# Optimization experiments

Measured on AMD Instinct MI355X. Metric: run time of the kernel, lower is better.

The kernel has to match this reference:

```python
import jax, jax.numpy as jnp
import numpy as np

D_MODEL = 1024
NHEAD = 16
D_K = D_MODEL // NHEAD
EPS_ATTN = 1e-6
EPS_LN = 1e-5


def _linear(k, fan_in, fan_out):
    k1, k2 = jax.random.split(k)
    bound = 1.0 / np.sqrt(fan_in)
    W = jax.random.uniform(k1, (fan_out, fan_in), jnp.float32, -bound, bound)
    b = jax.random.uniform(k2, (fan_out,), jnp.float32, -bound, bound)
    return W, b


def setup_inputs() -> dict:
    key = jax.random.key(0)
    ks = jax.random.split(key, 8)
    src = jax.random.normal(ks[0], (4096, 4, D_MODEL), jnp.float32)
    Wq, bq = _linear(ks[1], D_MODEL, D_MODEL)
    Wk, bk = _linear(ks[2], D_MODEL, D_MODEL)
    Wv, bv = _linear(ks[3], D_MODEL, D_MODEL)
    Wo, bo = _linear(ks[4], D_MODEL, D_MODEL)
    W1, b1 = _linear(ks[5], D_MODEL, 2 * D_MODEL)
    W2, b2 = _linear(ks[6], 2 * D_MODEL, D_MODEL)
    g1 = jnp.ones((D_MODEL,), jnp.float32)
    be1 = jnp.zeros((D_MODEL,), jnp.float32)
    g2 = jnp.ones((D_MODEL,), jnp.float32)
    be2 = jnp.zeros((D_MODEL,), jnp.float32)
    return {"src": src, "Wq": Wq, "bq": bq, "Wk": Wk, "bk": bk, "Wv": Wv, "bv": bv,
            "Wo": Wo, "bo": bo, "W1": W1, "b1": b1, "W2": W2, "b2": b2,
            "g1": g1, "be1": be1, "g2": g2, "be2": be2}


def _layernorm(x, g, b):
    mu = jnp.mean(x, axis=-1, keepdims=True)
    var = jnp.mean(jnp.square(x - mu), axis=-1, keepdims=True)
    return (x - mu) * jax.lax.rsqrt(var + EPS_LN) * g + b


def reference(src, Wq, bq, Wk, bk, Wv, bv, Wo, bo, W1, b1, W2, b2, g1, be1, g2, be2):
    S, B, D = src.shape
    Q = src @ Wq.T + bq  # [S,B,D]
    K = src @ Wk.T + bk
    V = src @ Wv.T + bv
    # split heads: [S,B,H,dk]
    Q = Q.reshape(S, B, NHEAD, D_K)
    K = K.reshape(S, B, NHEAD, D_K)
    V = V.reshape(S, B, NHEAD, D_K)
    phiQ = jax.nn.elu(Q) + 1.0
    phiK = jax.nn.elu(K) + 1.0
    # context per (batch, head): [B,H,dk,dk]
    context = jnp.einsum('sbhd,sbhe->bhde', phiK, V)
    out = jnp.einsum('sbhd,bhde->sbhe', phiQ, context)
    denom = jnp.einsum('sbhd,bhd->sbh', phiQ, phiK.sum(axis=0))
    out = out / (denom[..., None] + EPS_ATTN)
    attn = out.reshape(S, B, D)  # concat heads
    out = attn @ Wo.T + bo  # dropout = identity (eval)
    out = _layernorm(src + out, g1, be1)
    ffn = jax.nn.relu(out @ W1.T + b1) @ W2.T + b2
    out = _layernorm(out + ffn, g2, be2)
    return out
```

## Files before the change

kernel.cpp:

```cpp
#include <hip/hip_runtime.h>
#include <hip/hip_bf16.h>

typedef __hip_bfloat16 bf16;
typedef __attribute__((ext_vector_type(4))) float floatx4;
typedef __attribute__((ext_vector_type(8))) short shortx8;

#define MFMA16(a, b, c) __builtin_amdgcn_mfma_f32_16x16x32_bf16(a, b, c, 0, 0, 0)

__device__ __forceinline__ void gll16(const bf16* g, void* l) {
  __builtin_amdgcn_global_load_lds((const __attribute__((address_space(1))) unsigned int*)g,
                                   (__attribute__((address_space(3))) unsigned int*)l,
                                   16, 0, 0);
}

__device__ __forceinline__ float b2f(short s) {
  return __bfloat162float(__builtin_bit_cast(bf16, (unsigned short)s));
}
__device__ __forceinline__ short f2b(float f) {
  return __builtin_bit_cast(short, __float2bfloat16(f));
}

__global__ __launch_bounds__(256) void f2b_all(
    const float* __restrict__ src, const float* __restrict__ Wq,
    const float* __restrict__ Wk, const float* __restrict__ Wv,
    const float* __restrict__ Wo, const float* __restrict__ W1,
    const float* __restrict__ W2, bf16* __restrict__ src_bf,
    bf16* __restrict__ Wq_b, bf16* __restrict__ Wk_b, bf16* __restrict__ Wv_b,
    bf16* __restrict__ Wo_b, bf16* __restrict__ W1_b, bf16* __restrict__ W2_b) {
  const int blk = blockIdx.x;
  const float* in;
  bf16* out;
  int off;
  if (blk < 16384)      { in = src; out = src_bf; off = blk; }
  else if (blk < 17408) { in = Wq; out = Wq_b; off = blk - 16384; }
  else if (blk < 18432) { in = Wk; out = Wk_b; off = blk - 17408; }
  else if (blk < 19456) { in = Wv; out = Wv_b; off = blk - 18432; }
  else if (blk < 20480) { in = Wo; out = Wo_b; off = blk - 19456; }
  else if (blk < 22528) { in = W1; out = W1_b; off = blk - 20480; }
  else                  { in = W2; out = W2_b; off = blk - 22528; }
  const int i = (off * 256 + threadIdx.x) * 4;
  float4 v = *(const float4*)(in + i);
  ushort4 u;
  u.x = (unsigned short)f2b(v.x);
  u.y = (unsigned short)f2b(v.y);
  u.z = (unsigned short)f2b(v.z);
  u.w = (unsigned short)f2b(v.w);
  *(ushort4*)(out + i) = u;
}

template <int EPI>
__global__ __launch_bounds__(256, 2) void gemm_nt(
    const bf16* __restrict__ A, const bf16* __restrict__ Bw,
    const float* __restrict__ bias0, const float* __restrict__ bias1,
    const float* __restrict__ bias2, const float* __restrict__ resf,
    const bf16* __restrict__ resb, void* __restrict__ out0,
    void* __restrict__ out1, void* __restrict__ out2, const int M,
    const int K) {
  __shared__ __align__(16) char smem[24576];
  bf16* sA = (bf16*)smem;
  bf16* sB = (bf16*)(smem + 8192);
  bf16* cep = (bf16*)smem;
#define CEP(gg, rr, cc) cep[(((gg)*16 + (rr)) * 268) + (cc)]
  const int tid = threadIdx.x;
  const int lane = tid & 63, wave = tid >> 6;
  const int wm = wave & 1, wn = wave >> 1;
  const int bm = blockIdx.x, bn = blockIdx.y;
  floatx4 acc[4][8] = {};
  const int srow = tid >> 2;
  const int schunk = (tid & 3) ^ ((srow >> 1) & 3);
  const bf16* Ab = A + (size_t)(bm * 128 + srow) * K + schunk * 8;
  const bf16* Bb = Bw + (size_t)(bn * 256 + srow) * K + schunk * 8;
  const int woff = wave * 1024;
  const int frow = lane & 15;
  const int fks = (((lane >> 4) ^ ((frow >> 1) & 3))) << 3;
  const size_t rK = (size_t)64 * K;

  for (int k0 = 0; k0 < K; k0 += 32) {
    __syncthreads();
    gll16(Ab + k0, smem + woff);
    gll16(Ab + rK + k0, smem + 4096 + woff);
    gll16(Bb + k0, smem + 8192 + woff);
    gll16(Bb + rK + k0, smem + 12288 + woff);
    gll16(Bb + 2 * rK + k0, smem + 16384 + woff);
    gll16(Bb + 3 * rK + k0, smem + 20480 + woff);
    __syncthreads();
    shortx8 af[4], bfr[8];
#pragma unroll
    for (int i = 0; i < 4; i++)
      af[i] = *(const shortx8*)&sA[(wm * 64 + i * 16 + frow) * 32 + fks];
#pragma unroll
    for (int j = 0; j < 8; j++)
      bfr[j] = *(const shortx8*)&sB[(wn * 128 + j * 16 + frow) * 32 + fks];
#pragma unroll
    for (int i = 0; i < 4; i++)
#pragma unroll
      for (int j = 0; j < 8; j++)
        acc[i][j] = MFMA16(af[i], bfr[j], acc[i][j]);
  }

  const float* bptr = bias0;
  bf16* ob = (bf16*)out0;
  int colbase = bn * 256;
  int phi = 0;
  if (EPI == 4) {
    const int sel = bn >> 2;
    bptr = (sel == 0) ? bias0 : (sel == 1) ? bias1 : bias2;
    ob = (bf16*)((sel == 0) ? out0 : (sel == 1) ? out1 : out2);
    colbase = (bn & 3) * 256;
    phi = (sel < 2);
  }
  const int e = lane & 15, q4 = (lane >> 4) << 2;
  float bj[8];
#pragma unroll
  for (int j = 0; j < 8; j++) bj[j] = bptr[colbase + wn * 128 + j * 16 + e];

  const int g = tid >> 7;
  const int rowl = (tid >> 3) & 15;
  const int cch = (tid & 7) * 8;

#pragma unroll
  for (int i = 0; i < 4; i++) {
    __syncthreads();
#pragma unroll
    for (int j = 0; j < 8; j++) {
#pragma unroll
      for (int r = 0; r < 4; r++) {
        float v = acc[i][j][r] + bj[j];
        if (EPI == 4 && phi) v = v > 0.f ? v + 1.f : __expf(v);
        if (EPI == 2) v = fmaxf(v, 0.f);
        CEP(wm, q4 + r, wn * 128 + j * 16 + e) = __builtin_bit_cast(bf16, f2b(v));
      }
    }
    __syncthreads();
    const int grow = bm * 128 + g * 64 + i * 16 + rowl;
#pragma unroll
    for (int c = 0; c < 4; c++) {
      const int col = cch + c * 64;
      shortx8 v = *(const shortx8*)&CEP(g, rowl, col);
      if (EPI == 3) {
        const float* rp = resf + (size_t)grow * M + colbase + col;
        float4 r0 = *(const float4*)rp;
        float4 r1 = *(const float4*)(rp + 4);
        v[0] = f2b(b2f(v[0]) + r0.x); v[1] = f2b(b2f(v[1]) + r0.y);
        v[2] = f2b(b2f(v[2]) + r0.z); v[3] = f2b(b2f(v[3]) + r0.w);
        v[4] = f2b(b2f(v[4]) + r1.x); v[5] = f2b(b2f(v[5]) + r1.y);
        v[6] = f2b(b2f(v[6]) + r1.z); v[7] = f2b(b2f(v[7]) + r1.w);
      } else if (EPI == 5) {
        shortx8 rv = *(const shortx8*)(resb + (size_t)grow * M + colbase + col);
#pragma unroll
        for (int k = 0; k < 8; k++) v[k] = f2b(b2f(v[k]) + b2f(rv[k]));
      }
      *(shortx8*)(ob + (size_t)grow * M + colbase + col) = v;
    }
  }
#undef CEP
}

__global__ __launch_bounds__(256) void ctx_mfma(const bf16* __restrict__ phiK,
                                                const bf16* __restrict__ V,
                                                float* __restrict__ ctx,
                                                float* __restrict__ ksum) {
  __shared__ __align__(16) short sKT[64][72];
  __shared__ __align__(16) short sVT[64][72];
  const int bh = blockIdx.x, b = bh >> 4, h = bh & 15;
  const int t = threadIdx.x, lane = t & 63, wave = t >> 6;
  const int s_l = t >> 2;
  const int c0 = (t & 3) << 4;
  const int frow = lane & 15, fk = (lane >> 4) << 3;
  const shortx8 ones = (shortx8)(short)0x3F80;
  floatx4 acc[4] = {};
  floatx4 accK = {};

  const int sbeg = blockIdx.y * 512;
  for (int sub = 0; sub < 8; sub++) {
    const size_t g = ((size_t)(sbeg + sub * 64 + s_l) * 4 + b) * 1024 + h * 64 + c0;
    shortx8 kv0 = *(const shortx8*)(phiK + g);
    shortx8 kv1 = *(const shortx8*)(phiK + g + 8);
    shortx8 vv0 = *(const shortx8*)(V + g);
    shortx8 vv1 = *(const shortx8*)(V + g + 8);
    __syncthreads();
#pragma unroll
    for (int j = 0; j < 8; j++) {
      sKT[c0 + j][s_l] = kv0[j];
      sKT[c0 + 8 + j][s_l] = kv1[j];
      sVT[c0 + j][s_l] = vv0[j];
      sVT[c0 + 8 + j][s_l] = vv1[j];
    }
    __syncthreads();
#pragma unroll
    for (int ks = 0; ks < 2; ks++) {
      shortx8 af = *(const shortx8*)&sKT[wave * 16 + frow][ks * 32 + fk];
      accK = MFMA16(af, ones, accK);
#pragma unroll
      for (int j = 0; j < 4; j++) {
        shortx8 bfr = *(const shortx8*)&sVT[j * 16 + frow][ks * 32 + fk];
        acc[j] = MFMA16(af, bfr, acc[j]);
      }
    }
  }

  float* cdst = ctx + (size_t)bh * 4096;
  const int dr0 = wave * 16 + ((lane >> 4) << 2);
  const int e = lane & 15;
#pragma unroll
  for (int j = 0; j < 4; j++)
#pragma unroll
    for (int r = 0; r < 4; r++)
      atomicAdd(cdst + (size_t)(dr0 + r) * 64 + j * 16 + e, acc[j][r]);
  if (e == 0) {
#pragma unroll
    for (int r = 0; r < 4; r++) atomicAdd(ksum + bh * 64 + dr0 + r, accK[r]);
  }
}

__global__ __launch_bounds__(256) void attn_mfma(const bf16* __restrict__ phiQ,
                                                 const float* __restrict__ ctx,
                                                 const float* __restrict__ ksum,
                                                 bf16* __restrict__ attn) {
  __shared__ __align__(16) bf16 sctxT[64][72];
  __shared__ __align__(16) bf16 sks[64];
  const int bh = blockIdx.x, b = bh >> 4, h = bh & 15;
  const int t = threadIdx.x, lane = t & 63, wave = t >> 6;
  const float* cbase = ctx + (size_t)bh * 4096;
  for (int idx = t; idx < 4096; idx += 256) {
    int d = idx >> 6, e = idx & 63;
    sctxT[e][d] = __float2bfloat16(cbase[idx]);
  }
  if (t < 64) sks[t] = __float2bfloat16(ksum[bh * 64 + t]);
  __syncthreads();

  const int s0 = blockIdx.y * 128 + wave * 32;
  const int frow = lane & 15, fk = (lane >> 4) << 3;
  shortx8 bfr[2][4], kfr[2];
#pragma unroll
  for (int ks = 0; ks < 2; ks++) {
#pragma unroll
    for (int j = 0; j < 4; j++) bfr[ks][j] = *(const shortx8*)&sctxT[j * 16 + frow][ks * 32 + fk];
    kfr[ks] = *(const shortx8*)&sks[ks * 32 + fk];
  }
  floatx4 acc[2][4] = {};
  floatx4 accd[2] = {};
#pragma unroll
  for (int i = 0; i < 2; i++) {
#pragma unroll
    for (int ks = 0; ks < 2; ks++) {
      const int srow = s0 + i * 16 + frow;
      const bf16* ap = phiQ + ((size_t)srow * 4 + b) * 1024 + h * 64 + ks * 32 + fk;
      shortx8 af = *(const shortx8*)ap;
#pragma unroll
      for (int j = 0; j < 4; j++) acc[i][j] = MFMA16(af, bfr[ks][j], acc[i][j]);
      accd[i] = MFMA16(af, kfr[ks], accd[i]);
    }
  }
#pragma unroll
  for (int i = 0; i < 2; i++) {
#pragma unroll
    for (int r = 0; r < 4; r++) {
      const int srow = s0 + i * 16 + ((lane >> 4) << 2) + r;
      const float den = accd[i][r] + 1e-6f;
#pragma unroll
      for (int j = 0; j < 4; j++) {
        const int e = j * 16 + (lane & 15);
        attn[((size_t)srow * 4 + b) * 1024 + h * 64 + e] = __float2bfloat16(acc[i][j][r] / den);
      }
    }
  }
}

__global__ __launch_bounds__(256) void ln_kernel(const bf16* __restrict__ x,
                                                 const float* __restrict__ g,
                                                 const float* __restrict__ be,
                                                 bf16* __restrict__ outb,
                                                 float* __restrict__ outf) {
  const int row = blockIdx.x, t = threadIdx.x;
  const ushort4 u = ((const ushort4*)(x + (size_t)row * 1024))[t];
  float v0 = b2f((short)u.x), v1 = b2f((short)u.y);
  float v2 = b2f((short)u.z), v3 = b2f((short)u.w);
  float s = v0 + v1 + v2 + v3;
  float q = v0 * v0 + v1 * v1 + v2 * v2 + v3 * v3;
#pragma unroll
  for (int off = 32; off; off >>= 1) {
    s += __shfl_xor(s, off);
    q += __shfl_xor(q, off);
  }
  __shared__ float ss[4], sq[4];
  const int wave = t >> 6;
  if ((t & 63) == 0) { ss[wave] = s; sq[wave] = q; }
  __syncthreads();
  s = ss[0] + ss[1] + ss[2] + ss[3];
  q = sq[0] + sq[1] + sq[2] + sq[3];
  const float mu = s * (1.f / 1024.f);
  const float var = q * (1.f / 1024.f) - mu * mu;
  const float rstd = rsqrtf(var + 1e-5f);
  const float4 gv = ((const float4*)g)[t];
  const float4 bv = ((const float4*)be)[t];
  float y0 = (v0 - mu) * rstd * gv.x + bv.x;
  float y1 = (v1 - mu) * rstd * gv.y + bv.y;
  float y2 = (v2 - mu) * rstd * gv.z + bv.z;
  float y3 = (v3 - mu) * rstd * gv.w + bv.w;
  if (outb != nullptr) {
    ushort4 o;
    o.x = (unsigned short)f2b(y0); o.y = (unsigned short)f2b(y1);
    o.z = (unsigned short)f2b(y2); o.w = (unsigned short)f2b(y3);
    ((ushort4*)(outb + (size_t)row * 1024))[t] = o;
  } else {
    float4 o = {y0, y1, y2, y3};
    ((float4*)(outf + (size_t)row * 1024))[t] = o;
  }
}

extern "C" void kernel_launch(void* const* d_in, const int* in_sizes, int n_in,
                              void* d_out, int out_size, void* d_ws, size_t ws_size,
                              hipStream_t stream) {
  const float* src = (const float*)d_in[0];
  const float* Wq = (const float*)d_in[1];
  const float* bq = (const float*)d_in[2];
  const float* Wk = (const float*)d_in[3];
  const float* bk = (const float*)d_in[4];
  const float* Wv = (const float*)d_in[5];
  const float* bv = (const float*)d_in[6];
  const float* Wo = (const float*)d_in[7];
  const float* bo = (const float*)d_in[8];
  const float* W1 = (const float*)d_in[9];
  const float* b1 = (const float*)d_in[10];
  const float* W2 = (const float*)d_in[11];
  const float* b2 = (const float*)d_in[12];
  const float* g1 = (const float*)d_in[13];
  const float* be1 = (const float*)d_in[14];
  const float* g2 = (const float*)d_in[15];
  const float* be2 = (const float*)d_in[16];

  const size_t MB = 1024 * 1024;
  char* w = (char*)d_ws;
  bf16* src_bf = (bf16*)(w + 0);
  bf16* x1b = (bf16*)(w + 0);
  bf16* phiQ = (bf16*)(w + 64 * MB);
  bf16* phiK = (bf16*)(w + 96 * MB);
  bf16* attn = (bf16*)(w + 96 * MB);
  bf16* Vb = (bf16*)(w + 128 * MB);
  bf16* out1b = (bf16*)(w + 128 * MB);
  bf16* x2b = (bf16*)(w + 160 * MB);
  bf16* Wq_b = (bf16*)(w + 224 * MB);
  bf16* Wk_b = (bf16*)(w + 226 * MB);
  bf16* Wv_b = (bf16*)(w + 228 * MB);
  bf16* Wo_b = (bf16*)(w + 230 * MB);
  bf16* W1_b = (bf16*)(w + 232 * MB);
  bf16* W2_b = (bf16*)(w + 236 * MB);
  float* ctx = (float*)(w + 240 * MB);
  float* ksum = (float*)(w + 241 * MB);
  bf16* H1 = (bf16*)d_out;
  float* outf = (float*)d_out;

  const dim3 blk(256);
  f2b_all<<<24576, blk, 0, stream>>>(src, Wq, Wk, Wv, Wo, W1, W2, src_bf, Wq_b,
                                     Wk_b, Wv_b, Wo_b, W1_b, W2_b);
  hipMemsetAsync(ctx, 0, (64 * 64 * 64 + 64 * 64) * sizeof(float), stream);

  gemm_nt<4><<<dim3(128, 12), blk, 0, stream>>>(
      src_bf, Wq_b, bq, bk, bv, nullptr, nullptr, phiQ, phiK, Vb, 1024, 1024);
  ctx_mfma<<<dim3(64, 8), blk, 0, stream>>>(phiK, Vb, ctx, ksum);
  attn_mfma<<<dim3(64, 32), blk, 0, stream>>>(phiQ, ctx, ksum, attn);
  gemm_nt<3><<<dim3(128, 4), blk, 0, stream>>>(
      attn, Wo_b, bo, nullptr, nullptr, src, nullptr, x1b, nullptr, nullptr, 1024, 1024);
  ln_kernel<<<16384, blk, 0, stream>>>(x1b, g1, be1, out1b, nullptr);
  gemm_nt<2><<<dim3(128, 8), blk, 0, stream>>>(
      out1b, W1_b, b1, nullptr, nullptr, nullptr, nullptr, H1, nullptr, nullptr, 2048, 1024);
  gemm_nt<5><<<dim3(128, 4), blk, 0, stream>>>(
      H1, W2_b, b2, nullptr, nullptr, nullptr, out1b, x2b, nullptr, nullptr, 1024, 2048);
  ln_kernel<<<16384, blk, 0, stream>>>(x2b, g2, be2, nullptr, outf);
}
```

Measured before the change: 567.5 us.

## Replace GEMM with 256x256-tile, 4-stage LDS-pipelined 512-thread kernel

Replaces the 128x256 single-buffered GEMM with a 256x256 tile run by 8 waves. The new kernel uses a 4-deep ring of LDS stages filled by global_load_lds, with explicit vmcnt and lgkmcnt waits, raw barriers and setprio around the MFMA bursts. The goal is to overlap global loads with MFMA work and to double operand reuse per tile, cutting the per-k-step barrier stalls of the old kernel. The cost is 128KB of LDS per block, which likely limits each CU to one block. It also means fewer blocks, for example 256 blocks for the N=1024 GEMMs, which raises the risk of wave-quantization and tail effects.

```diff
diff --git a/kernel.cpp b/kernel.cpp
--- a/kernel.cpp
+++ b/kernel.cpp
@@ -11,6 +11,13 @@
   __builtin_amdgcn_global_load_lds((const __attribute__((address_space(1))) unsigned int*)g,
                                    (__attribute__((address_space(3))) unsigned int*)l,
                                    16, 0, 0);
+}
+
+__device__ __forceinline__ shortx8 ds8(const char* p) {
+  shortx8 r;
+  unsigned a = (unsigned)(unsigned long long)(const __attribute__((address_space(3))) char*)p;
+  asm volatile("ds_read_b128 %0, %1" : "=v"(r) : "v"(a));
+  return r;
 }
 
 __device__ __forceinline__ float b2f(short s) {
@@ -49,55 +56,104 @@
 }
 
 template <int EPI>
-__global__ __launch_bounds__(256, 2) void gemm_nt(
+__global__ __launch_bounds__(512, 2) void gemm256(
     const bf16* __restrict__ A, const bf16* __restrict__ Bw,
     const float* __restrict__ bias0, const float* __restrict__ bias1,
     const float* __restrict__ bias2, const float* __restrict__ resf,
     const bf16* __restrict__ resb, void* __restrict__ out0,
     void* __restrict__ out1, void* __restrict__ out2, const int M,
     const int K) {
-  __shared__ __align__(16) char smem[24576];
-  bf16* sA = (bf16*)smem;
-  bf16* sB = (bf16*)(smem + 8192);
-  bf16* cep = (bf16*)smem;
-#define CEP(gg, rr, cc) cep[(((gg)*16 + (rr)) * 268) + (cc)]
+  __shared__ __align__(16) char smem[131072];
   const int tid = threadIdx.x;
   const int lane = tid & 63, wave = tid >> 6;
   const int wm = wave & 1, wn = wave >> 1;
   const int bm = blockIdx.x, bn = blockIdx.y;
-  floatx4 acc[4][8] = {};
+  const int NK = K >> 5;
+
   const int srow = tid >> 2;
   const int schunk = (tid & 3) ^ ((srow >> 1) & 3);
-  const bf16* Ab = A + (size_t)(bm * 128 + srow) * K + schunk * 8;
-  const bf16* Bb = Bw + (size_t)(bn * 256 + srow) * K + schunk * 8;
-  const int woff = wave * 1024;
+  const bf16* gA0 = A + (size_t)(bm * 256 + srow) * K + schunk * 8;
+  const bf16* gA1 = gA0 + (size_t)128 * K;
+  const bf16* gB0 = Bw + (size_t)(bn * 256 + srow) * K + schunk * 8;
+  const bf16* gB1 = gB0 + (size_t)128 * K;
+  const unsigned ldst = (unsigned)wave * 1024u;
+
   const int frow = lane & 15;
-  const int fks = (((lane >> 4) ^ ((frow >> 1) & 3))) << 3;
-  const size_t rK = (size_t)64 * K;
-
-  for (int k0 = 0; k0 < K; k0 += 32) {
-    __syncthreads();
-    gll16(Ab + k0, smem + woff);
-    gll16(Ab + rK + k0, smem + 4096 + woff);
-    gll16(Bb + k0, smem + 8192 + woff);
-    gll16(Bb + rK + k0, smem + 12288 + woff);
-    gll16(Bb + 2 * rK + k0, smem + 16384 + woff);
-    gll16(Bb + 3 * rK + k0, smem + 20480 + woff);
-    __syncthreads();
-    shortx8 af[4], bfr[8];
+  const unsigned fch16 = (unsigned)(((lane >> 4) ^ ((frow >> 1) & 3))) << 4;
+  const unsigned aoff0 = (unsigned)(wm * 8192 + frow * 64) + fch16;
+  const unsigned boff0 = 65536u + (unsigned)(wn * 4096 + frow * 64) + fch16;
+
+  floatx4 acc[8][4] = {};
+
+#define STAGE_A(t)                                                       \
+  {                                                                      \
+    const int kk = (t) * 32;                                             \
+    const unsigned bo = (unsigned)(((t) & 3) * 16384) + ldst;            \
+    gll16(gA0 + kk, smem + bo);                                          \
+    gll16(gA1 + kk, smem + bo + 8192);                                   \
+  }
+#define STAGE_B(t)                                                       \
+  {                                                                      \
+    const int kk = (t) * 32;                                             \
+    const unsigned bo = 65536u + (unsigned)(((t) & 3) * 16384) + ldst;   \
+    gll16(gB0 + kk, smem + bo);                                          \
+    gll16(gB1 + kk, smem + bo + 8192);                                   \
+  }
+
+  STAGE_A(0); STAGE_B(0);
+  STAGE_A(1); STAGE_B(1);
+  STAGE_A(2); STAGE_B(2);
+  asm volatile("s_waitcnt vmcnt(8)");
+  __builtin_amdgcn_sched_barrier(0);
+  __builtin_amdgcn_s_barrier();
+
+  for (int kt = 0; kt < NK; ++kt) {
+    const unsigned ab = aoff0 + (unsigned)((kt & 3) * 16384);
+    const unsigned bb = boff0 + (unsigned)((kt & 3) * 16384);
+    shortx8 bfr[4], af[4];
+#pragma unroll
+    for (int j = 0; j < 4; j++) bfr[j] = ds8(smem + bb + j * 1024);
+#pragma unroll
+    for (int i = 0; i < 4; i++) af[i] = ds8(smem + ab + i * 1024);
+    if (kt + 3 < NK) STAGE_A(kt + 3);
+    __builtin_amdgcn_s_barrier();
+    asm volatile("s_waitcnt lgkmcnt(0)");
+    __builtin_amdgcn_sched_barrier(0);
+    __builtin_amdgcn_s_setprio(1);
 #pragma unroll
     for (int i = 0; i < 4; i++)
-      af[i] = *(const shortx8*)&sA[(wm * 64 + i * 16 + frow) * 32 + fks];
-#pragma unroll
-    for (int j = 0; j < 8; j++)
-      bfr[j] = *(const shortx8*)&sB[(wn * 128 + j * 16 + frow) * 32 + fks];
+#pragma unroll
+      for (int j = 0; j < 4; j++) acc[i][j] = MFMA16(af[i], bfr[j], acc[i][j]);
+    __builtin_amdgcn_s_setprio(0);
+#pragma unroll
+    for (int i = 0; i < 4; i++) af[i] = ds8(smem + ab + (4 + i) * 1024);
+    if (kt + 3 < NK) STAGE_B(kt + 3);
+    __builtin_amdgcn_s_barrier();
+    asm volatile("s_waitcnt lgkmcnt(0)");
+    __builtin_amdgcn_sched_barrier(0);
+    __builtin_amdgcn_s_setprio(1);
 #pragma unroll
     for (int i = 0; i < 4; i++)
 #pragma unroll
-      for (int j = 0; j < 8; j++)
-        acc[i][j] = MFMA16(af[i], bfr[j], acc[i][j]);
-  }
-
+      for (int j = 0; j < 4; j++)
+        acc[4 + i][j] = MFMA16(af[i], bfr[j], acc[4 + i][j]);
+    __builtin_amdgcn_s_setprio(0);
+    if (kt < NK - 1) {
+      if (kt < NK - 3) {
+        asm volatile("s_waitcnt vmcnt(8)");
+      } else if (kt == NK - 3) {
+        asm volatile("s_waitcnt vmcnt(4)");
+      } else {
+        asm volatile("s_waitcnt vmcnt(0)");
+      }
+      __builtin_amdgcn_sched_barrier(0);
+      __builtin_amdgcn_s_barrier();
+    }
+  }
+#undef STAGE_A
+#undef STAGE_B
+
+  bf16* cep = (bf16*)smem;
   const float* bptr = bias0;
   bf16* ob = (bf16*)out0;
   int colbase = bn * 256;
@@ -110,33 +166,33 @@
     phi = (sel < 2);
   }
   const int e = lane & 15, q4 = (lane >> 4) << 2;
-  float bj[8];
-#pragma unroll
-  for (int j = 0; j < 8; j++) bj[j] = bptr[colbase + wn * 128 + j * 16 + e];
-
-  const int g = tid >> 7;
-  const int rowl = (tid >> 3) & 15;
-  const int cch = (tid & 7) * 8;
-
-#pragma unroll
-  for (int i = 0; i < 4; i++) {
+  float bj[4];
+#pragma unroll
+  for (int j = 0; j < 4; j++) bj[j] = bptr[colbase + wn * 64 + j * 16 + e];
+
+  const int ridx = tid >> 4;
+  const int cc = (tid & 15) * 8;
+  const int grow_base = bm * 256 + (ridx >> 4) * 128 + (ridx & 15);
+
+#pragma unroll
+  for (int i = 0; i < 8; i++) {
     __syncthreads();
 #pragma unroll
-    for (int j = 0; j < 8; j++) {
+    for (int j = 0; j < 4; j++)
 #pragma unroll
       for (int r = 0; r < 4; r++) {
         float v = acc[i][j][r] + bj[j];
         if (EPI == 4 && phi) v = v > 0.f ? v + 1.f : __expf(v);
         if (EPI == 2) v = fmaxf(v, 0.f);
-        CEP(wm, q4 + r, wn * 128 + j * 16 + e) = __builtin_bit_cast(bf16, f2b(v));
+        cep[(wm * 16 + q4 + r) * 264 + wn * 64 + j * 16 + e] =
+            __builtin_bit_cast(bf16, f2b(v));
       }
-    }
     __syncthreads();
-    const int grow = bm * 128 + g * 64 + i * 16 + rowl;
-#pragma unroll
-    for (int c = 0; c < 4; c++) {
-      const int col = cch + c * 64;
-      shortx8 v = *(const shortx8*)&CEP(g, rowl, col);
+    const int grow = grow_base + i * 16;
+#pragma unroll
+    for (int h = 0; h < 2; h++) {
+      const int col = cc + h * 128;
+      shortx8 v = *(const shortx8*)&cep[ridx * 264 + col];
       if (EPI == 3) {
         const float* rp = resf + (size_t)grow * M + colbase + col;
         float4 r0 = *(const float4*)rp;
@@ -153,7 +209,6 @@
       *(shortx8*)(ob + (size_t)grow * M + colbase + col) = v;
     }
   }
-#undef CEP
 }
 
 __global__ __launch_bounds__(256) void ctx_mfma(const bf16* __restrict__ phiK,
@@ -351,21 +406,21 @@
   bf16* H1 = (bf16*)d_out;
   float* outf = (float*)d_out;
 
-  const dim3 blk(256);
+  const dim3 blk(256), blk5(512);
   f2b_all<<<24576, blk, 0, stream>>>(src, Wq, Wk, Wv, Wo, W1, W2, src_bf, Wq_b,
                                      Wk_b, Wv_b, Wo_b, W1_b, W2_b);
   hipMemsetAsync(ctx, 0, (64 * 64 * 64 + 64 * 64) * sizeof(float), stream);
 
-  gemm_nt<4><<<dim3(128, 12), blk, 0, stream>>>(
+  gemm256<4><<<dim3(64, 12), blk5, 0, stream>>>(
       src_bf, Wq_b, bq, bk, bv, nullptr, nullptr, phiQ, phiK, Vb, 1024, 1024);
   ctx_mfma<<<dim3(64, 8), blk, 0, stream>>>(phiK, Vb, ctx, ksum);
   attn_mfma<<<dim3(64, 32), blk, 0, stream>>>(phiQ, ctx, ksum, attn);
-  gemm_nt<3><<<dim3(128, 4), blk, 0, stream>>>(
+  gemm256<3><<<dim3(64, 4), blk5, 0, stream>>>(
       attn, Wo_b, bo, nullptr, nullptr, src, nullptr, x1b, nullptr, nullptr, 1024, 1024);
   ln_kernel<<<16384, blk, 0, stream>>>(x1b, g1, be1, out1b, nullptr);
-  gemm_nt<2><<<dim3(128, 8), blk, 0, stream>>>(
+  gemm256<2><<<dim3(64, 8), blk5, 0, stream>>>(
       out1b, W1_b, b1, nullptr, nullptr, nullptr, nullptr, H1, nullptr, nullptr, 2048, 1024);
-  gemm_nt<5><<<dim3(128, 4), blk, 0, stream>>>(
+  gemm256<5><<<dim3(64, 4), blk5, 0, stream>>>(
       H1, W2_b, b2, nullptr, nullptr, nullptr, out1b, x2b, nullptr, nullptr, 1024, 2048);
   ln_kernel<<<16384, blk, 0, stream>>>(x2b, g2, be2, nullptr, outf);
 }
```

Result: faster. 532.8 us (-6.1%).

## Rewrite GEMM as 256x128-tile, 512-thread kernel with double-buffered LDS prefetch

Applied to the files above, without the earlier changes.

Replaces the 128x256-tile, 256-thread GEMM with a 256x128-tile kernel run by 8 waves, each computing a 64x64 sub-tile. K-slices are double-buffered in 48 KB of LDS, so the next slice's global-to-LDS load is issued before the current slice's MFMAs and only one barrier per iteration is needed. The epilogue is rewritten to stage 32 rows at a time through LDS. Costs are more LDS per block and fewer accumulator registers per wave, with a risk of lower occupancy and more epilogue barriers.

```diff
diff --git a/kernel.cpp b/kernel.cpp
--- a/kernel.cpp
+++ b/kernel.cpp
@@ -49,111 +49,122 @@
 }
 
 template <int EPI>
-__global__ __launch_bounds__(256, 2) void gemm_nt(
+__global__ __launch_bounds__(512, 4) void gemm128(
     const bf16* __restrict__ A, const bf16* __restrict__ Bw,
     const float* __restrict__ bias0, const float* __restrict__ bias1,
     const float* __restrict__ bias2, const float* __restrict__ resf,
     const bf16* __restrict__ resb, void* __restrict__ out0,
     void* __restrict__ out1, void* __restrict__ out2, const int M,
     const int K) {
-  __shared__ __align__(16) char smem[24576];
-  bf16* sA = (bf16*)smem;
-  bf16* sB = (bf16*)(smem + 8192);
-  bf16* cep = (bf16*)smem;
-#define CEP(gg, rr, cc) cep[(((gg)*16 + (rr)) * 268) + (cc)]
+  __shared__ __align__(16) char smem[49152];
   const int tid = threadIdx.x;
   const int lane = tid & 63, wave = tid >> 6;
-  const int wm = wave & 1, wn = wave >> 1;
+  const int wm = wave >> 1, wn = wave & 1;
   const int bm = blockIdx.x, bn = blockIdx.y;
-  floatx4 acc[4][8] = {};
+  const int NK = K >> 5;
+
   const int srow = tid >> 2;
   const int schunk = (tid & 3) ^ ((srow >> 1) & 3);
-  const bf16* Ab = A + (size_t)(bm * 128 + srow) * K + schunk * 8;
-  const bf16* Bb = Bw + (size_t)(bn * 256 + srow) * K + schunk * 8;
-  const int woff = wave * 1024;
+  const bf16* gA0 = A + (size_t)(bm * 256 + srow) * K + schunk * 8;
+  const bf16* gA1 = gA0 + (size_t)128 * K;
+  const bf16* gB0 = Bw + (size_t)(bn * 128 + srow) * K + schunk * 8;
+  const unsigned ldst = (unsigned)wave * 1024u;
+
   const int frow = lane & 15;
-  const int fks = (((lane >> 4) ^ ((frow >> 1) & 3))) << 3;
-  const size_t rK = (size_t)64 * K;
-
-  for (int k0 = 0; k0 < K; k0 += 32) {
-    __syncthreads();
-    gll16(Ab + k0, smem + woff);
-    gll16(Ab + rK + k0, smem + 4096 + woff);
-    gll16(Bb + k0, smem + 8192 + woff);
-    gll16(Bb + rK + k0, smem + 12288 + woff);
-    gll16(Bb + 2 * rK + k0, smem + 16384 + woff);
-    gll16(Bb + 3 * rK + k0, smem + 20480 + woff);
-    __syncthreads();
-    shortx8 af[4], bfr[8];
+  const unsigned fch16 = (unsigned)(((lane >> 4) ^ ((frow >> 1) & 3))) << 4;
+  const unsigned aoffW =
+      (unsigned)((wm >> 1) * 8192) + (unsigned)(((wm & 1) * 64 + frow) * 64) + fch16;
+  const unsigned boffW = 16384u + (unsigned)((wn * 64 + frow) * 64) + fch16;
+
+  floatx4 acc[4][4] = {};
+
+#define STAGE(t)                                                         \
+  {                                                                      \
+    const int kk = (t) * 32;                                             \
+    const unsigned so = (unsigned)(((t) & 1) * 24576);                   \
+    gll16(gA0 + kk, smem + so + ldst);                                   \
+    gll16(gA1 + kk, smem + so + 8192 + ldst);                            \
+    gll16(gB0 + kk, smem + so + 16384 + ldst);                           \
+  }
+
+  STAGE(0);
+  __syncthreads();
+
+  for (int kt = 0; kt < NK; ++kt) {
+    const unsigned so = (unsigned)((kt & 1) * 24576);
+    if (kt + 1 < NK) STAGE(kt + 1);
+    shortx8 afr[4], bfr[4];
 #pragma unroll
     for (int i = 0; i < 4; i++)
-      af[i] = *(const shortx8*)&sA[(wm * 64 + i * 16 + frow) * 32 + fks];
-#pragma unroll
-    for (int j = 0; j < 8; j++)
-      bfr[j] = *(const shortx8*)&sB[(wn * 128 + j * 16 + frow) * 32 + fks];
+      afr[i] = *(const shortx8*)(smem + so + aoffW + i * 1024);
+#pragma unroll
+    for (int j = 0; j < 4; j++)
+      bfr[j] = *(const shortx8*)(smem + so + boffW + j * 1024);
 #pragma unroll
     for (int i = 0; i < 4; i++)
 #pragma unroll
-      for (int j = 0; j < 8; j++)
-        acc[i][j] = MFMA16(af[i], bfr[j], acc[i][j]);
-  }
-
+      for (int j = 0; j < 4; j++) acc[i][j] = MFMA16(afr[i], bfr[j], acc[i][j]);
+    __syncthreads();
+  }
+#undef STAGE
+
+  bf16* cep = (bf16*)smem;
   const float* bptr = bias0;
   bf16* ob = (bf16*)out0;
-  int colbase = bn * 256;
+  int colbase = bn * 128;
   int phi = 0;
   if (EPI == 4) {
-    const int sel = bn >> 2;
+    const int sel = bn >> 3;
     bptr = (sel == 0) ? bias0 : (sel == 1) ? bias1 : bias2;
     ob = (bf16*)((sel == 0) ? out0 : (sel == 1) ? out1 : out2);
-    colbase = (bn & 3) * 256;
+    colbase = (bn & 7) * 128;
     phi = (sel < 2);
   }
   const int e = lane & 15, q4 = (lane >> 4) << 2;
-  float bj[8];
-#pragma unroll
-  for (int j = 0; j < 8; j++) bj[j] = bptr[colbase + wn * 128 + j * 16 + e];
-
-  const int g = tid >> 7;
-  const int rowl = (tid >> 3) & 15;
-  const int cch = (tid & 7) * 8;
-
-#pragma unroll
-  for (int i = 0; i < 4; i++) {
-    __syncthreads();
-#pragma unroll
-    for (int j = 0; j < 8; j++) {
-#pragma unroll
-      for (int r = 0; r < 4; r++) {
-        float v = acc[i][j][r] + bj[j];
-        if (EPI == 4 && phi) v = v > 0.f ? v + 1.f : __expf(v);
-        if (EPI == 2) v = fmaxf(v, 0.f);
-        CEP(wm, q4 + r, wn * 128 + j * 16 + e) = __builtin_bit_cast(bf16, f2b(v));
+  float bj[4];
+#pragma unroll
+  for (int j = 0; j < 4; j++) bj[j] = bptr[colbase + wn * 64 + j * 16 + e];
+
+  const int ridx = tid >> 4;
+  const int cc = (tid & 15) * 8;
+
+#pragma unroll
+  for (int s3 = 0; s3 < 8; s3++) {
+    __syncthreads();
+    if (wm == (s3 >> 1)) {
+#pragma unroll
+      for (int ii = 0; ii < 2; ii++) {
+        const int i2 = (s3 & 1) * 2 + ii;
+#pragma unroll
+        for (int j = 0; j < 4; j++)
+#pragma unroll
+          for (int r = 0; r < 4; r++) {
+            float v = acc[i2][j][r] + bj[j];
+            if (EPI == 4 && phi) v = v > 0.f ? v + 1.f : __expf(v);
+            if (EPI == 2) v = fmaxf(v, 0.f);
+            cep[(ii * 16 + q4 + r) * 134 + wn * 64 + j * 16 + e] =
+                __builtin_bit_cast(bf16, f2b(v));
+          }
       }
     }
     __syncthreads();
-    const int grow = bm * 128 + g * 64 + i * 16 + rowl;
-#pragma unroll
-    for (int c = 0; c < 4; c++) {
-      const int col = cch + c * 64;
-      shortx8 v = *(const shortx8*)&CEP(g, rowl, col);
-      if (EPI == 3) {
-        const float* rp = resf + (size_t)grow * M + colbase + col;
-        float4 r0 = *(const float4*)rp;
-        float4 r1 = *(const float4*)(rp + 4);
-        v[0] = f2b(b2f(v[0]) + r0.x); v[1] = f2b(b2f(v[1]) + r0.y);
-        v[2] = f2b(b2f(v[2]) + r0.z); v[3] = f2b(b2f(v[3]) + r0.w);
-        v[4] = f2b(b2f(v[4]) + r1.x); v[5] = f2b(b2f(v[5]) + r1.y);
-        v[6] = f2b(b2f(v[6]) + r1.z); v[7] = f2b(b2f(v[7]) + r1.w);
-      } else if (EPI == 5) {
-        shortx8 rv = *(const shortx8*)(resb + (size_t)grow * M + colbase + col);
-#pragma unroll
-        for (int k = 0; k < 8; k++) v[k] = f2b(b2f(v[k]) + b2f(rv[k]));
-      }
-      *(shortx8*)(ob + (size_t)grow * M + colbase + col) = v;
-    }
-  }
-#undef CEP
+    const int grow = bm * 256 + s3 * 32 + ridx;
+    shortx8 v = *(const shortx8*)&cep[ridx * 134 + cc];
+    if (EPI == 3) {
+      const float* rp = resf + (size_t)grow * M + colbase + cc;
+      float4 r0 = *(const float4*)rp;
+      float4 r1 = *(const float4*)(rp + 4);
+      v[0] = f2b(b2f(v[0]) + r0.x); v[1] = f2b(b2f(v[1]) + r0.y);
+      v[2] = f2b(b2f(v[2]) + r0.z); v[3] = f2b(b2f(v[3]) + r0.w);
+      v[4] = f2b(b2f(v[4]) + r1.x); v[5] = f2b(b2f(v[5]) + r1.y);
+      v[6] = f2b(b2f(v[6]) + r1.z); v[7] = f2b(b2f(v[7]) + r1.w);
+    } else if (EPI == 5) {
+      shortx8 rv = *(const shortx8*)(resb + (size_t)grow * M + colbase + cc);
+#pragma unroll
+      for (int k = 0; k < 8; k++) v[k] = f2b(b2f(v[k]) + b2f(rv[k]));
+    }
+    *(shortx8*)(ob + (size_t)grow * M + colbase + cc) = v;
+  }
 }
 
 __global__ __launch_bounds__(256) void ctx_mfma(const bf16* __restrict__ phiK,
@@ -351,21 +362,21 @@
   bf16* H1 = (bf16*)d_out;
   float* outf = (float*)d_out;
 
-  const dim3 blk(256);
+  const dim3 blk(256), blk5(512);
   f2b_all<<<24576, blk, 0, stream>>>(src, Wq, Wk, Wv, Wo, W1, W2, src_bf, Wq_b,
                                      Wk_b, Wv_b, Wo_b, W1_b, W2_b);
   hipMemsetAsync(ctx, 0, (64 * 64 * 64 + 64 * 64) * sizeof(float), stream);
 
-  gemm_nt<4><<<dim3(128, 12), blk, 0, stream>>>(
+  gemm128<4><<<dim3(64, 24), blk5, 0, stream>>>(
       src_bf, Wq_b, bq, bk, bv, nullptr, nullptr, phiQ, phiK, Vb, 1024, 1024);
   ctx_mfma<<<dim3(64, 8), blk, 0, stream>>>(phiK, Vb, ctx, ksum);
   attn_mfma<<<dim3(64, 32), blk, 0, stream>>>(phiQ, ctx, ksum, attn);
-  gemm_nt<3><<<dim3(128, 4), blk, 0, stream>>>(
+  gemm128<3><<<dim3(64, 8), blk5, 0, stream>>>(
       attn, Wo_b, bo, nullptr, nullptr, src, nullptr, x1b, nullptr, nullptr, 1024, 1024);
   ln_kernel<<<16384, blk, 0, stream>>>(x1b, g1, be1, out1b, nullptr);
-  gemm_nt<2><<<dim3(128, 8), blk, 0, stream>>>(
+  gemm128<2><<<dim3(64, 16), blk5, 0, stream>>>(
       out1b, W1_b, b1, nullptr, nullptr, nullptr, nullptr, H1, nullptr, nullptr, 2048, 1024);
-  gemm_nt<5><<<dim3(128, 4), blk, 0, stream>>>(
+  gemm128<5><<<dim3(64, 8), blk5, 0, stream>>>(
       H1, W2_b, b2, nullptr, nullptr, nullptr, out1b, x2b, nullptr, nullptr, 1024, 2048);
   ln_kernel<<<16384, blk, 0, stream>>>(x2b, g2, be2, nullptr, outf);
 }
```

New measurement: 569.3 us. No clear change (+0.3%).
